# Optimization experiments

Hardware: AMD Instinct MI355X
Metric: run time of the kernel (lower is better)

## Reference

```python
import jax, jax.numpy as jnp
import numpy as np

B, S, D_IN, D_OUT = 8, 2048, 1024, 64

def setup_inputs() -> dict:
    key = jax.random.key(0)
    ks = jax.random.split(key, 6)
    return {
        "inputs_for_keys": jax.random.normal(ks[0], (B, S, D_IN), jnp.float32),
        "inputs_for_values": jax.random.normal(ks[1], (B, S, D_IN), jnp.float32),
        "inputs_for_queries": jax.random.normal(ks[2], (B, S, D_IN), jnp.float32),
        "K": jax.random.normal(ks[3], (D_IN, D_OUT), jnp.float32) * (1.0 / np.sqrt(D_IN)),
        "V": jax.random.normal(ks[4], (D_IN, D_OUT), jnp.float32) * (1.0 / np.sqrt(D_IN)),
        "Q": jax.random.normal(ks[5], (D_IN, D_OUT), jnp.float32) * (1.0 / np.sqrt(D_IN)),
    }

def reference(inputs_for_keys, inputs_for_values, inputs_for_queries, K, V, Q):
    # Project to per-head key/value/query spaces: [B, S, D_OUT]
    keys = jnp.einsum('bsd,de->bse', inputs_for_keys, K)
    values = jnp.einsum('bsd,de->bse', inputs_for_values, V)
    queries = jnp.einsum('bsd,de->bse', inputs_for_queries, Q)
    d_k = keys.shape[-1]
    # Scaled dot-product scores: [B, Sq, Sk]
    score = jnp.einsum('bqe,bke->bqk', queries, keys) / jnp.sqrt(jnp.float32(d_k))
    # Causal mask: -inf strictly above the diagonal (query i attends to keys <= i)
    sq, sk = score.shape[1], score.shape[2]
    causal = jnp.triu(jnp.full((sq, sk), -jnp.inf, dtype=score.dtype), k=1)
    score = score + causal[None, :, :]
    weights = jax.nn.softmax(score, axis=-1)
    # Attention output: [B, Sq, D_OUT]
    return jnp.einsum('bqk,bke->bqe', weights, values)
```

## Files before the change

kernel.cpp:

```cpp
#include <hip/hip_runtime.h>
#include <stdint.h>

#define BB   8
#define SS   2048
#define DIN  1024
#define DOUT 64

typedef __bf16 bf16_t;
typedef __bf16 bf16x4 __attribute__((ext_vector_type(4)));
typedef __bf16 bf16x8 __attribute__((ext_vector_type(8)));
typedef float  f32x4  __attribute__((ext_vector_type(4)));
typedef unsigned int u32x4 __attribute__((ext_vector_type(4)));

#define LOG2E 1.44269504088896f

__device__ __forceinline__ void load_lds16(const void* g, void* l) {
    __builtin_amdgcn_global_load_lds(
        (const __attribute__((address_space(1))) void*)g,
        (__attribute__((address_space(3))) void*)l, 16, 0, 0);
}

__global__ void prep_weights(const float* __restrict__ Kw,
                             const float* __restrict__ Vw,
                             const float* __restrict__ Qw,
                             bf16_t* __restrict__ fw) {
    int proj = blockIdx.x >> 4;
    int seg  = blockIdx.x & 15;
    const float* W = (proj == 0) ? Kw : (proj == 1) ? Vw : Qw;
    float scale = (proj == 2) ? 0.125f : 1.0f;
    bf16_t* out = fw + proj * 65536;
    int base = seg * 4096;
#pragma unroll
    for (int i = 0; i < 16; ++i) {
        int idx  = base + i * 256 + threadIdx.x;
        int j    = idx & 7;
        int lane = (idx >> 3) & 63;
        int nt   = (idx >> 9) & 3;
        int kk   = idx >> 11;
        int k    = kk * 32 + (lane >> 4) * 8 + j;
        int col  = nt * 16 + (lane & 15);
        out[idx] = (bf16_t)(W[k * DOUT + col] * scale);
    }
}

__global__ __launch_bounds__(256) void proj_kernel(
    const float* __restrict__ Xk, const float* __restrict__ Xv,
    const float* __restrict__ Xq, const bf16_t* __restrict__ fw,
    bf16_t* __restrict__ outK, bf16_t* __restrict__ outVT,
    bf16_t* __restrict__ outQ) {
    __shared__ __align__(128) char Ab[3][8192];
    __shared__ __align__(128) char Bb[3][8192];

    int tid  = threadIdx.x;
    int lane = tid & 63;
    int w    = tid >> 6;

    int proj = blockIdx.y;
    const float* X  = (proj == 0) ? Xk : (proj == 1) ? Xv : Xq;
    bf16_t* out     = (proj == 0) ? outK : (proj == 1) ? outVT : outQ;
    const bf16_t* fwp = fw + proj * 65536;

    int row0 = blockIdx.x * 32;

    const float* ga = X + (size_t)(row0 + (tid >> 4)) * DIN + ((tid & 15) ^ (tid >> 4)) * 4;

    f32x4 acc0 = (f32x4)(0.0f), acc1 = (f32x4)(0.0f);
    int r   = (w & 1) * 16 + (lane & 15);
    int nt0 = (w >> 1) * 2;

#define STAGE(kt, b) do {                                                   \
        load_lds16(ga + (kt) * 64,            Ab[b] + (w << 10));           \
        load_lds16(ga + 16 * DIN + (kt) * 64, Ab[b] + 4096 + (w << 10));    \
        load_lds16(fwp + (kt) * 4096 + tid * 8,        Bb[b] + (w << 10));  \
        load_lds16(fwp + (kt) * 4096 + 2048 + tid * 8, Bb[b] + 4096 + (w << 10)); \
    } while (0)

#define COMPUTE(b) do {                                                     \
        _Pragma("unroll")                                                   \
        for (int s = 0; s < 2; ++s) {                                       \
            int b0 = s * 8 + (lane >> 4) * 2;                               \
            f32x4 lo = *(const f32x4*)(Ab[b] + r * 256 + (((b0    ) ^ (lane & 15)) << 4)); \
            f32x4 hi = *(const f32x4*)(Ab[b] + r * 256 + (((b0 + 1) ^ (lane & 15)) << 4)); \
            bf16x8 af;                                                      \
            af[0] = (bf16_t)lo[0]; af[1] = (bf16_t)lo[1];                   \
            af[2] = (bf16_t)lo[2]; af[3] = (bf16_t)lo[3];                   \
            af[4] = (bf16_t)hi[0]; af[5] = (bf16_t)hi[1];                   \
            af[6] = (bf16_t)hi[2]; af[7] = (bf16_t)hi[3];                   \
            bf16x8 bf0 = *(const bf16x8*)(Bb[b] + s * 4096 + nt0 * 1024 + lane * 16); \
            bf16x8 bf1 = *(const bf16x8*)(Bb[b] + s * 4096 + (nt0 + 1) * 1024 + lane * 16); \
            acc0 = __builtin_amdgcn_mfma_f32_16x16x32_bf16(af, bf0, acc0, 0, 0, 0); \
            acc1 = __builtin_amdgcn_mfma_f32_16x16x32_bf16(af, bf1, acc1, 0, 0, 0); \
        }                                                                   \
    } while (0)

    STAGE(0, 0);
    STAGE(1, 1);

#pragma unroll
    for (int t = 0; t < 16; ++t) {
        if (t + 2 < 16) STAGE(t + 2, (t + 2) % 3);
        if (t < 14)       asm volatile("s_waitcnt vmcnt(8)" ::: "memory");
        else if (t == 14) asm volatile("s_waitcnt vmcnt(4)" ::: "memory");
        else              asm volatile("s_waitcnt vmcnt(0)" ::: "memory");
        __builtin_amdgcn_s_barrier();
        COMPUTE(t % 3);
        __builtin_amdgcn_s_barrier();
    }
#undef STAGE
#undef COMPUTE

    if (proj != 1) {
#pragma unroll
        for (int j = 0; j < 4; ++j) {
            int orow = row0 + (w & 1) * 16 + (lane >> 4) * 4 + j;
            out[(size_t)orow * DOUT + nt0 * 16 + (lane & 15)]       = (bf16_t)acc0[j];
            out[(size_t)orow * DOUT + (nt0 + 1) * 16 + (lane & 15)] = (bf16_t)acc1[j];
        }
    } else {
        char* Al = &Ab[0][0];
#pragma unroll
        for (int j = 0; j < 4; ++j) {
            int row = (w & 1) * 16 + (lane >> 4) * 4 + j;
            int c0  = nt0 * 16 + (lane & 15);
            int c1  = c0 + 16;
            *(bf16_t*)(Al + row * 128 + ((c0 * 2) ^ ((row & 7) << 4))) = (bf16_t)acc0[j];
            *(bf16_t*)(Al + row * 128 + ((c1 * 2) ^ ((row & 7) << 4))) = (bf16_t)acc1[j];
        }
        __syncthreads();
        int b  = row0 >> 11;
        int s0 = row0 & 2047;
        int sl = tid & 31;
        int d0 = (tid >> 5) * 8;
        bf16_t vals[8];
#pragma unroll
        for (int j = 0; j < 8; ++j)
            vals[j] = *(const bf16_t*)(Al + sl * 128 + (((d0 + j) * 2) ^ ((sl & 7) << 4)));
#pragma unroll
        for (int j = 0; j < 8; ++j)
            out[(size_t)b * (DOUT * SS) + (size_t)(d0 + j) * SS + s0 + sl] = vals[j];
    }
}

__global__ __launch_bounds__(256) void attn_kernel(
    const bf16_t* __restrict__ Kp, const bf16_t* __restrict__ VpT,
    const bf16_t* __restrict__ Qp, float* __restrict__ out,
    float* __restrict__ Opart, float* __restrict__ Oml, int split) {
    __shared__ __align__(16) char Plds[4][2048];

    int tid  = threadIdx.x;
    int lane = tid & 63;
    int w    = tid >> 6;
    int idx  = blockIdx.x;
    int b    = blockIdx.y;

    int qt, t0, t1, half = 0;
    bool partial;
    if (!split || idx < 16) { qt = idx; t0 = 0; t1 = qt + 1; partial = false; }
    else {
        int e = idx - 16;
        qt   = 16 + (e >> 1);
        half = e & 1;
        int T = qt + 1, h = (T + 1) >> 1;
        t0 = half ? h : 0;
        t1 = half ? T : h;
        partial = true;
    }

    const bf16_t* Kb = Kp  + (size_t)b * SS * DOUT;
    const bf16_t* Vb = VpT + (size_t)b * DOUT * SS;
    const bf16_t* Qb = Qp  + (size_t)b * SS * DOUT;

    bf16x8 aq0, aq1;
    {
        int rq = qt * 64 + w * 16 + (lane & 15);
        const bf16_t* qp = Qb + (size_t)rq * DOUT + (lane >> 4) * 8;
        aq0 = *(const bf16x8*)(qp);
        aq1 = *(const bf16x8*)(qp + 32);
    }

    float m[4], lsum[4];
    f32x4 acc[4];
#pragma unroll
    for (int r = 0; r < 4; ++r) { m[r] = -1e30f; lsum[r] = 0.0f; }
#pragma unroll
    for (int nt = 0; nt < 4; ++nt) acc[nt] = (f32x4)(0.0f);

    char* Pw = &Plds[w][0];

    for (int t = t0; t < t1; ++t) {
        f32x4 sfr[4];
#pragma unroll
        for (int nt = 0; nt < 4; ++nt) sfr[nt] = (f32x4)(0.0f);
#pragma unroll
        for (int kk = 0; kk < 2; ++kk) {
            int d0 = kk * 32 + (lane >> 4) * 8;
#pragma unroll
            for (int nt = 0; nt < 4; ++nt) {
                int key = nt * 16 + (lane & 15);
                bf16x8 bk = *(const bf16x8*)(Kb + (size_t)(t * 64 + key) * DOUT + d0);
                sfr[nt] = __builtin_amdgcn_mfma_f32_16x16x32_bf16(
                              kk == 0 ? aq0 : aq1, bk, sfr[nt], 0, 0, 0);
            }
        }

        if (t == qt) {
#pragma unroll
            for (int nt = 0; nt < 4; ++nt) {
                int key = nt * 16 + (lane & 15);
#pragma unroll
                for (int r = 0; r < 4; ++r) {
                    int q = w * 16 + (lane >> 4) * 4 + r;
                    if (key > q) sfr[nt][r] = -1e30f;
                }
            }
        }

        float pf[4][4];
#pragma unroll
        for (int r = 0; r < 4; ++r) {
            float mx = fmaxf(fmaxf(sfr[0][r], sfr[1][r]), fmaxf(sfr[2][r], sfr[3][r]));
            mx = fmaxf(mx, __shfl_xor(mx, 1));
            mx = fmaxf(mx, __shfl_xor(mx, 2));
            mx = fmaxf(mx, __shfl_xor(mx, 4));
            mx = fmaxf(mx, __shfl_xor(mx, 8));
            float mn = fmaxf(m[r], mx);
            float scale = exp2f((m[r] - mn) * LOG2E);
            m[r] = mn;
            float rs = 0.0f;
#pragma unroll
            for (int nt = 0; nt < 4; ++nt) {
                float p = exp2f((sfr[nt][r] - mn) * LOG2E);
                pf[nt][r] = p;
                rs += p;
            }
            rs += __shfl_xor(rs, 1);
            rs += __shfl_xor(rs, 2);
            rs += __shfl_xor(rs, 4);
            rs += __shfl_xor(rs, 8);
            lsum[r] = lsum[r] * scale + rs;
#pragma unroll
            for (int nt = 0; nt < 4; ++nt) acc[nt][r] *= scale;
        }

#pragma unroll
        for (int nt = 0; nt < 4; ++nt) {
            int key = nt * 16 + (lane & 15);
#pragma unroll
            for (int r = 0; r < 4; ++r) {
                int q = (lane >> 4) * 4 + r;
                *(bf16_t*)(Pw + q * 128 + ((key * 2) ^ ((q & 7) << 4))) = (bf16_t)pf[nt][r];
            }
        }

#pragma unroll
        for (int kk = 0; kk < 2; ++kk) {
            int k0 = kk * 32 + (lane >> 4) * 8;
            int q  = lane & 15;
            bf16x8 ap = *(const bf16x8*)(Pw + q * 128 + ((k0 * 2) ^ ((q & 7) << 4)));
#pragma unroll
            for (int nt = 0; nt < 4; ++nt) {
                int d = nt * 16 + (lane & 15);
                bf16x8 bv = *(const bf16x8*)(Vb + (size_t)d * SS + t * 64 + k0);
                acc[nt] = __builtin_amdgcn_mfma_f32_16x16x32_bf16(ap, bv, acc[nt], 0, 0, 0);
            }
        }
    }

    if (!partial) {
        float* ob = out + ((size_t)b * SS + qt * 64 + w * 16) * DOUT;
#pragma unroll
        for (int nt = 0; nt < 4; ++nt)
#pragma unroll
            for (int r = 0; r < 4; ++r) {
                int q = (lane >> 4) * 4 + r;
                int d = nt * 16 + (lane & 15);
                ob[(size_t)q * DOUT + d] = acc[nt][r] / lsum[r];
            }
    } else {
        size_t pbase = (((size_t)b * 16 + (qt - 16)) * 2 + half);
        float* Op = Opart + pbase * 4096;
        float* Ml = Oml   + pbase * 128;
#pragma unroll
        for (int nt = 0; nt < 4; ++nt)
#pragma unroll
            for (int r = 0; r < 4; ++r) {
                int row = w * 16 + (lane >> 4) * 4 + r;
                Op[row * 64 + nt * 16 + (lane & 15)] = acc[nt][r];
            }
        if ((lane & 15) == 0) {
#pragma unroll
            for (int r = 0; r < 4; ++r) {
                int row = w * 16 + (lane >> 4) * 4 + r;
                Ml[row * 2]     = m[r];
                Ml[row * 2 + 1] = lsum[r];
            }
        }
    }
}

__global__ __launch_bounds__(256) void attn_combine(
    const float* __restrict__ Opart, const float* __restrict__ Oml,
    float* __restrict__ out) {
    int qt  = 16 + blockIdx.x;
    int b   = blockIdx.y;
    int tid = threadIdx.x;
    int row = tid >> 2;
    int cb  = (tid & 3) * 16;

    size_t base = ((size_t)b * 16 + (qt - 16)) * 2;
    const float* O0 = Opart + base * 4096;
    const float* O1 = O0 + 4096;
    const float* M0 = Oml + base * 128;
    const float* M1 = M0 + 128;

    float m0 = M0[row * 2], l0 = M0[row * 2 + 1];
    float m1 = M1[row * 2], l1 = M1[row * 2 + 1];
    float mm = fmaxf(m0, m1);
    float e0 = exp2f((m0 - mm) * LOG2E);
    float e1 = exp2f((m1 - mm) * LOG2E);
    float li = 1.0f / (l0 * e0 + l1 * e1);

    const float* p0 = O0 + row * 64 + cb;
    const float* p1 = O1 + row * 64 + cb;
    float* ob = out + ((size_t)b * SS + qt * 64 + row) * DOUT + cb;
#pragma unroll
    for (int i = 0; i < 4; ++i) {
        f32x4 a = *(const f32x4*)(p0 + i * 4);
        f32x4 c = *(const f32x4*)(p1 + i * 4);
        f32x4 o;
#pragma unroll
        for (int j = 0; j < 4; ++j) o[j] = (a[j] * e0 + c[j] * e1) * li;
        *(f32x4*)(ob + i * 4) = o;
    }
}

extern "C" void kernel_launch(void* const* d_in, const int* in_sizes, int n_in,
                              void* d_out, int out_size, void* d_ws, size_t ws_size,
                              hipStream_t stream) {
    const float* Xk = (const float*)d_in[0];
    const float* Xv = (const float*)d_in[1];
    const float* Xq = (const float*)d_in[2];
    const float* Kw = (const float*)d_in[3];
    const float* Vw = (const float*)d_in[4];
    const float* Qw = (const float*)d_in[5];

    bf16_t* Kp  = (bf16_t*)d_ws;
    bf16_t* VpT = Kp  + (size_t)BB * SS * DOUT;
    bf16_t* Qp  = VpT + (size_t)BB * SS * DOUT;
    bf16_t* fw  = Qp  + (size_t)BB * SS * DOUT;
    char*   pend = (char*)(fw + 3 * 65536);
    float*  Opart = (float*)pend;
    float*  Oml   = Opart + (size_t)8 * 16 * 2 * 4096;

    size_t need = (size_t)((char*)(Oml + 8 * 16 * 2 * 128) - (char*)d_ws);
    int split = (ws_size >= need) ? 1 : 0;

    prep_weights<<<dim3(48), dim3(256), 0, stream>>>(Kw, Vw, Qw, fw);
    proj_kernel<<<dim3(512, 3), dim3(256), 0, stream>>>(Xk, Xv, Xq, fw, Kp, VpT, Qp);
    attn_kernel<<<dim3(split ? 48 : 32, 8), dim3(256), 0, stream>>>(
        Kp, VpT, Qp, (float*)d_out, Opart, Oml, split);
    if (split)
        attn_combine<<<dim3(16, 8), dim3(256), 0, stream>>>(Opart, Oml, (float*)d_out);
}
```

Before: 107.8 us.

## Split projection into fp32-to-bf16 conversion pass and bf16 MFMA GEMM

Adds a kernel that converts the three fp32 input activations to bf16 in workspace, followed by a simpler bf16 GEMM kernel that loads a 16-row tile into LDS and multiplies by the pre-swizzled weights. The aim is to simplify the GEMM's load pipeline and conversion work. In exchange it adds an extra full write and re-read of the activations. The new path is used only when the workspace is large enough, otherwise it falls back to the fused proj_kernel.

```diff
diff --git a/kernel.cpp b/kernel.cpp
--- a/kernel.cpp
+++ b/kernel.cpp
@@ -43,6 +43,83 @@
     }
 }
 
+__global__ __launch_bounds__(256) void convert_kernel(
+    const float* __restrict__ Xk, const float* __restrict__ Xv,
+    const float* __restrict__ Xq, bf16_t* __restrict__ Xb) {
+    int proj = blockIdx.y;
+    const float* X = (proj == 0) ? Xk : (proj == 1) ? Xv : Xq;
+    bf16_t* O = Xb + (size_t)proj * ((size_t)BB * SS * DIN);
+    size_t e0 = (size_t)blockIdx.x * 8192;
+    int t = threadIdx.x;
+    const float* src = X + e0;
+    bf16_t* dst = O + e0;
+    f32x4 v[8];
+#pragma unroll
+    for (int i = 0; i < 8; ++i)
+        v[i] = *(const f32x4*)(src + i * 1024 + t * 4);
+#pragma unroll
+    for (int i = 0; i < 8; ++i) {
+        bf16x4 o;
+        o[0] = (bf16_t)v[i][0]; o[1] = (bf16_t)v[i][1];
+        o[2] = (bf16_t)v[i][2]; o[3] = (bf16_t)v[i][3];
+        *(bf16x4*)(dst + i * 1024 + t * 4) = o;
+    }
+}
+
+__global__ __launch_bounds__(256) void gemm_bf16(
+    const bf16_t* __restrict__ Xb, const bf16_t* __restrict__ fw,
+    bf16_t* __restrict__ outK, bf16_t* __restrict__ outVT,
+    bf16_t* __restrict__ outQ) {
+    __shared__ __align__(128) char Al[32768];
+
+    int tid  = threadIdx.x;
+    int lane = tid & 63;
+    int w    = tid >> 6;
+
+    int proj = blockIdx.y;
+    const bf16_t* Xp  = Xb + (size_t)proj * ((size_t)BB * SS * DIN);
+    const bf16_t* fwp = fw + proj * 65536;
+
+    int row0 = blockIdx.x * 16;
+    const char* xbase = (const char*)(Xp + (size_t)row0 * DIN);
+
+#pragma unroll
+    for (int i = 0; i < 8; ++i) {
+        int L   = i * 256 + tid;
+        int row = L >> 7;
+        int pos = L & 127;
+        load_lds16(xbase + row * 2048 + ((pos ^ (row & 15)) << 4),
+                   Al + i * 4096 + (w << 10));
+    }
+    __syncthreads();
+
+    f32x4 acc = (f32x4)(0.0f);
+    int arow = lane & 15;
+    int hi   = lane >> 4;
+#pragma unroll 8
+    for (int kk = 0; kk < 32; ++kk) {
+        int blk = kk * 4 + hi;
+        bf16x8 a = *(const bf16x8*)(Al + arow * 2048 + ((blk ^ arow) << 4));
+        bf16x8 b = *(const bf16x8*)(fwp + kk * 2048 + w * 512 + lane * 8);
+        acc = __builtin_amdgcn_mfma_f32_16x16x32_bf16(a, b, acc, 0, 0, 0);
+    }
+
+    if (proj != 1) {
+        bf16_t* out = (proj == 0) ? outK : outQ;
+#pragma unroll
+        for (int j = 0; j < 4; ++j)
+            out[(size_t)(row0 + hi * 4 + j) * DOUT + w * 16 + arow] = (bf16_t)acc[j];
+    } else {
+        int b  = row0 >> 11;
+        int s0 = row0 & 2047;
+        bf16x4 o;
+        o[0] = (bf16_t)acc[0]; o[1] = (bf16_t)acc[1];
+        o[2] = (bf16_t)acc[2]; o[3] = (bf16_t)acc[3];
+        *(bf16x4*)(outVT + (size_t)b * DOUT * SS +
+                   (size_t)(w * 16 + arow) * SS + s0 + hi * 4) = o;
+    }
+}
+
 __global__ __launch_bounds__(256) void proj_kernel(
     const float* __restrict__ Xk, const float* __restrict__ Xv,
     const float* __restrict__ Xq, const bf16_t* __restrict__ fw,
@@ -61,7 +138,6 @@
     const bf16_t* fwp = fw + proj * 65536;
 
     int row0 = blockIdx.x * 32;
-
     const float* ga = X + (size_t)(row0 + (tid >> 4)) * DIN + ((tid & 15) ^ (tid >> 4)) * 4;
 
     f32x4 acc0 = (f32x4)(0.0f), acc1 = (f32x4)(0.0f);
@@ -95,7 +171,6 @@
 
     STAGE(0, 0);
     STAGE(1, 1);
-
 #pragma unroll
     for (int t = 0; t < 16; ++t) {
         if (t + 2 < 16) STAGE(t + 2, (t + 2) % 3);
@@ -117,14 +192,14 @@
             out[(size_t)orow * DOUT + (nt0 + 1) * 16 + (lane & 15)] = (bf16_t)acc1[j];
         }
     } else {
-        char* Al = &Ab[0][0];
+        char* Al2 = &Ab[0][0];
 #pragma unroll
         for (int j = 0; j < 4; ++j) {
             int row = (w & 1) * 16 + (lane >> 4) * 4 + j;
             int c0  = nt0 * 16 + (lane & 15);
             int c1  = c0 + 16;
-            *(bf16_t*)(Al + row * 128 + ((c0 * 2) ^ ((row & 7) << 4))) = (bf16_t)acc0[j];
-            *(bf16_t*)(Al + row * 128 + ((c1 * 2) ^ ((row & 7) << 4))) = (bf16_t)acc1[j];
+            *(bf16_t*)(Al2 + row * 128 + ((c0 * 2) ^ ((row & 7) << 4))) = (bf16_t)acc0[j];
+            *(bf16_t*)(Al2 + row * 128 + ((c1 * 2) ^ ((row & 7) << 4))) = (bf16_t)acc1[j];
         }
         __syncthreads();
         int b  = row0 >> 11;
@@ -134,7 +209,7 @@
         bf16_t vals[8];
 #pragma unroll
         for (int j = 0; j < 8; ++j)
-            vals[j] = *(const bf16_t*)(Al + sl * 128 + (((d0 + j) * 2) ^ ((sl & 7) << 4)));
+            vals[j] = *(const bf16_t*)(Al2 + sl * 128 + (((d0 + j) * 2) ^ ((sl & 7) << 4)));
 #pragma unroll
         for (int j = 0; j < 8; ++j)
             out[(size_t)b * (DOUT * SS) + (size_t)(d0 + j) * SS + s0 + sl] = vals[j];
@@ -349,14 +424,30 @@
     bf16_t* Qp  = VpT + (size_t)BB * SS * DOUT;
     bf16_t* fw  = Qp  + (size_t)BB * SS * DOUT;
     char*   pend = (char*)(fw + 3 * 65536);
-    float*  Opart = (float*)pend;
-    float*  Oml   = Opart + (size_t)8 * 16 * 2 * 4096;
-
-    size_t need = (size_t)((char*)(Oml + 8 * 16 * 2 * 128) - (char*)d_ws);
-    int split = (ws_size >= need) ? 1 : 0;
+
+    size_t xb_bytes = (size_t)3 * BB * SS * DIN * 2;
+    size_t base_off = (size_t)(pend - (char*)d_ws);
+    bool full = ws_size >= base_off + xb_bytes;
 
     prep_weights<<<dim3(48), dim3(256), 0, stream>>>(Kw, Vw, Qw, fw);
-    proj_kernel<<<dim3(512, 3), dim3(256), 0, stream>>>(Xk, Xv, Xq, fw, Kp, VpT, Qp);
+
+    float* Opart;
+    float* Oml;
+    if (full) {
+        bf16_t* Xb = (bf16_t*)pend;
+        Opart = (float*)pend;
+        Oml   = Opart + (size_t)8 * 16 * 2 * 4096;
+        convert_kernel<<<dim3(2048, 3), dim3(256), 0, stream>>>(Xk, Xv, Xq, Xb);
+        gemm_bf16<<<dim3(1024, 3), dim3(256), 0, stream>>>(Xb, fw, Kp, VpT, Qp);
+    } else {
+        Opart = (float*)pend;
+        Oml   = Opart + (size_t)8 * 16 * 2 * 4096;
+        proj_kernel<<<dim3(512, 3), dim3(256), 0, stream>>>(Xk, Xv, Xq, fw, Kp, VpT, Qp);
+    }
+
+    size_t need_split = base_off + (size_t)8 * 16 * 2 * (4096 + 128) * 4;
+    int split = (ws_size >= need_split) ? 1 : 0;
+
     attn_kernel<<<dim3(split ? 48 : 32, 8), dim3(256), 0, stream>>>(
         Kp, VpT, Qp, (float*)d_out, Opart, Oml, split);
     if (split)
```

After: 144.2 us. 33.8% more time.
